# Kernel optimization log

Hardware: AMD Instinct MI355X
Metric: run time of the kernel (lower is better)

The kernel has to match this reference:

```python
import jax, jax.numpy as jnp
import numpy as np

RRELU_SLOPE = (1.0 / 8.0 + 1.0 / 3.0) / 2.0  # F.rrelu deterministic (eval) slope

N_ENTS, H_DIM, R2, T, E = 50000, 200, 500, 4, 400000


def setup_inputs() -> dict:
    key = jax.random.key(0)
    ks = jax.random.split(key, 16)
    s = 0.05
    inp = {
        # learned parameters
        "dynamic_emb": jax.random.normal(ks[0], (N_ENTS, H_DIM), jnp.float32),
        "emb_rel": jax.random.normal(ks[1], (R2, H_DIM), jnp.float32) * s,
        "W_ih": jax.random.normal(ks[2], (3 * H_DIM, 2 * H_DIM), jnp.float32) * s,
        "W_hh": jax.random.normal(ks[3], (3 * H_DIM, H_DIM), jnp.float32) * s,
        "b_ih": jnp.zeros((3 * H_DIM,), jnp.float32),
        "b_hh": jnp.zeros((3 * H_DIM,), jnp.float32),
        "weight_neighbor": jax.random.normal(ks[4], (H_DIM, H_DIM), jnp.float32) * s,
        "time_gate_weight": jax.random.normal(ks[5], (H_DIM, H_DIM), jnp.float32) * s,
        "time_gate_bias": jnp.zeros((H_DIM,), jnp.float32),
        # per-timestep graph structure [T, E]
        "src": jax.random.randint(ks[6], (T, E), 0, N_ENTS, jnp.int32),
        "dst": jax.random.randint(ks[7], (T, E), 0, N_ENTS, jnp.int32),
        "etype": jax.random.randint(ks[8], (T, E), 0, R2, jnp.int32),
        "r_to_e": jax.random.randint(ks[9], (T, E), 0, N_ENTS, jnp.int32),
        "r_seg": jnp.sort(jax.random.randint(ks[10], (T, E), 0, R2, jnp.int32), axis=1),
    }
    return inp


def _l2norm(x):
    # torch F.normalize along dim=1
    return x / jnp.maximum(jnp.linalg.norm(x, axis=1, keepdims=True), 1e-12)


def reference(dynamic_emb, emb_rel, W_ih, W_hh, b_ih, b_hh, weight_neighbor,
              time_gate_weight, time_gate_bias, src, dst, etype, r_to_e, r_seg):
    N, H = dynamic_emb.shape
    R2_ = emb_rel.shape[0]

    def gru(x, hprev):
        gi = x @ W_ih.T + b_ih
        gh = hprev @ W_hh.T + b_hh
        ir, iz, inn = jnp.split(gi, 3, axis=1)
        hr, hz, hn = jnp.split(gh, 3, axis=1)
        r = jax.nn.sigmoid(ir + hr)
        z = jax.nn.sigmoid(iz + hz)
        n = jnp.tanh(inn + r * hn)
        return (1.0 - z) * n + z * hprev

    def rgcn(h, s, d, et):
        # UnionRGCNLayer: msg = (h_src + rel_emb[etype]) @ W_neighbor, sum-agg, 1/deg norm, rrelu
        msg = (h[s] + emb_rel[et]) @ weight_neighbor  # [E, H]
        agg = jax.ops.segment_sum(msg, d, num_segments=N)
        deg = jax.ops.segment_sum(jnp.ones((s.shape[0],), h.dtype), d, num_segments=N)
        norm = jnp.where(deg > 0, 1.0 / jnp.maximum(deg, 1.0), 0.0)
        out = agg * norm[:, None]
        return jnp.where(out >= 0, out, RRELU_SLOPE * out)

    h_init = _l2norm(dynamic_emb)  # layer_norm=True

    def step(carry, g):
        h, h0 = carry
        s, d, et, rte, rseg = g
        # ragged per-relation segment mean of entity embeddings
        temp = h[rte]  # [E, H]
        sums = jax.ops.segment_sum(temp, rseg, num_segments=R2_)
        cnts = jax.ops.segment_sum(jnp.ones((rte.shape[0],), h.dtype), rseg, num_segments=R2_)
        x_input = jnp.where(cnts[:, None] > 0, sums / jnp.maximum(cnts, 1.0)[:, None], 0.0)
        x_cat = jnp.concatenate([emb_rel, x_input], axis=1)  # [R2, 2H]
        h0_new = _l2norm(gru(x_cat, h0))
        cur = _l2norm(rgcn(h, s, d, et))
        tw = jax.nn.sigmoid(h @ time_gate_weight + time_gate_bias)
        h_new = _l2norm(tw * cur + (1.0 - tw) * h)
        return (h_new, h0_new), h_new

    (h_fin, h0_fin), evolve = jax.lax.scan(
        step, (h_init, emb_rel), (src, dst, etype, r_to_e, r_seg))
    return evolve, h0_fin  # evolve: [T, N, H]; h0: [2*num_rels, H]
```

## Files before the change

### kernel.cpp

```cpp
#include <hip/hip_runtime.h>
#include <hip/hip_bf16.h>

using bf16 = __hip_bfloat16;

constexpr int NE  = 50000;
constexpr int H   = 200;
constexpr int R2C = 500;
constexpr int TS  = 4;
constexpr int EC  = 400000;
constexpr float SLOPE = 0.22916666666666666f;
constexpr int NSCAN = (NE + 255) / 256;

constexpr int KP = 224;
constexpr int KS = 7;
constexpr int NT = 13;

constexpr int GNT = 38;
constexpr int GKI = 13;
constexpr int GKH = 7;
constexpr int GR  = 512;
constexpr int GCS = 608;

constexpr int RCH = 64;
constexpr int NRNG = 8;
constexpr int DRNG = NE / NRNG;
constexpr int SCHK = 1024;
constexpr int NCHK = (EC + SCHK - 1) / SCHK;
constexpr int GSCAT1 = NCHK * NRNG;

constexpr int GB_GEMM  = (NE + 63) / 64;
constexpr int GB_RELS  = EC / RCH;
constexpr int GB_AGG   = (NE + 3) / 4;
constexpr int GB_A2B   = (GR * 416 + GR * 224 + 255) / 256;

constexpr int PB_INITH  = (NE + 3) / 4;
constexpr int PB_INITH0 = (R2C * H + 255) / 256;
constexpr int PB_RELW   = R2C;
constexpr int PB_PACKB  = (2 * NT * KS * 64 + 255) / 256;
constexpr int PB_PACKG  = (GNT * (GKI + GKH) * 64 + 255) / 256;
constexpr int PB_SEGB   = TS;
constexpr int PB_ZS     = (TS * R2C * H + 255) / 256;
constexpr int PB_ZI     = (TS * NE + 255) / 256;
constexpr int PO0 = PB_INITH;
constexpr int PO1 = PO0 + PB_INITH0;
constexpr int PO2 = PO1 + PB_RELW;
constexpr int PO3 = PO2 + PB_PACKB;
constexpr int PO4 = PO3 + PB_PACKG;
constexpr int PO5 = PO4 + PB_SEGB;
constexpr int PO6 = PO5 + PB_ZS;
constexpr int PO7 = PO6 + PB_ZI;

#define DEVINL __device__ __forceinline__

typedef __bf16 bf16x8v __attribute__((ext_vector_type(8)));
typedef float  f32x4   __attribute__((ext_vector_type(4)));

DEVINL float b2f(bf16 v) { return __bfloat162float(v); }
DEVINL bf16  f2b(float v) { return __float2bfloat16(v); }
DEVINL unsigned short f2bu(float x) { bf16 b = f2b(x); return *reinterpret_cast<unsigned short*>(&b); }
DEVINL float u2f(unsigned short u) { unsigned int w = (unsigned int)u << 16; float f; __builtin_memcpy(&f, &w, 4); return f; }

DEVINL float wave_sum(float v) {
  #pragma unroll
  for (int o = 32; o > 0; o >>= 1) v += __shfl_xor(v, o, 64);
  return v;
}

DEVINL float sigmoidf(float x) { return 1.0f / (1.0f + expf(-x)); }


DEVINL void inith_body(int b, const float* __restrict__ de, float* __restrict__ h,
                       unsigned short* __restrict__ hb0) {
  int wid = threadIdx.x >> 6, lane = threadIdx.x & 63;
  int row = b * 4 + wid;
  if (row >= NE) return;
  int d0 = lane * 4;
  bool act = d0 < H;
  float4 v = make_float4(0.f, 0.f, 0.f, 0.f);
  if (act) v = *reinterpret_cast<const float4*>(de + (size_t)row * H + d0);
  float ss = v.x * v.x + v.y * v.y + v.z * v.z + v.w * v.w;
  ss = wave_sum(ss);
  float sc = 1.0f / fmaxf(sqrtf(ss), 1e-12f);
  if (act) {
    float4 o = make_float4(v.x * sc, v.y * sc, v.z * sc, v.w * sc);
    *reinterpret_cast<float4*>(h + (size_t)row * H + d0) = o;
    ushort4 ob; ob.x = f2bu(o.x); ob.y = f2bu(o.y); ob.z = f2bu(o.z); ob.w = f2bu(o.w);
    *reinterpret_cast<ushort4*>(hb0 + (size_t)row * KP + d0) = ob;
  } else if (d0 < KP) {
    ushort4 z; z.x = z.y = z.z = z.w = 0;
    *reinterpret_cast<ushort4*>(hb0 + (size_t)row * KP + d0) = z;
  }
}

DEVINL void inith0_body(int b, const float* er, float* h0) {
  int i = b * 256 + threadIdx.x;
  if (i < R2C * H) h0[i] = er[i];
}

DEVINL void relw_body(int b, const float* er, const float* wn, unsigned short* relWb) {
  __shared__ float a[H];
  int r = b;
  for (int d = threadIdx.x; d < H; d += 256) a[d] = er[r * H + d];
  __syncthreads();
  for (int c = threadIdx.x; c < H; c += 256) {
    float s = 0.f;
    for (int k = 0; k < H; k++) s += a[k] * wn[k * H + c];
    relWb[r * H + c] = f2bu(s);
  }
}

DEVINL void packb_body(int b, const float* wn, const float* tg, unsigned short* bpack) {
  int t = b * 256 + threadIdx.x;
  int total = 2 * NT * KS * 64;
  if (t >= total) return;
  int m    = t / (NT * KS * 64);
  int rem  = t % (NT * KS * 64);
  int nt   = rem / (KS * 64);
  int rem2 = rem % (KS * 64);
  int ks   = rem2 / 64, lane = rem2 % 64;
  const float* W = m ? tg : wn;
  int n = nt * 16 + (lane & 15);
  unsigned short out[8];
  #pragma unroll
  for (int j = 0; j < 8; j++) {
    int k = ks * 32 + (lane >> 4) * 8 + j;
    float v = (k < H && n < H) ? W[k * H + n] : 0.f;
    out[j] = f2bu(v);
  }
  unsigned short* dst = bpack + (size_t)t * 8;
  #pragma unroll
  for (int j = 0; j < 8; j++) dst[j] = out[j];
}

DEVINL void packgru_body(int b, const float* __restrict__ wih, const float* __restrict__ whh,
                         unsigned short* __restrict__ bgi, unsigned short* __restrict__ bgh) {
  int t = b * 256 + threadIdx.x;
  const int tot_i = GNT * GKI * 64;
  const int tot_h = GNT * GKH * 64;
  if (t < tot_i) {
    int nt = t / (GKI * 64);
    int rem = t % (GKI * 64);
    int ks = rem / 64, lane = rem % 64;
    int n = nt * 16 + (lane & 15);
    unsigned short o[8];
    #pragma unroll
    for (int j = 0; j < 8; j++) {
      int k = ks * 32 + (lane >> 4) * 8 + j;
      o[j] = (n < 3 * H && k < 2 * H) ? f2bu(wih[n * (2 * H) + k]) : (unsigned short)0;
    }
    unsigned short* dstp = bgi + (size_t)t * 8;
    #pragma unroll
    for (int j = 0; j < 8; j++) dstp[j] = o[j];
  } else if (t < tot_i + tot_h) {
    int t2 = t - tot_i;
    int nt = t2 / (GKH * 64);
    int rem = t2 % (GKH * 64);
    int ks = rem / 64, lane = rem % 64;
    int n = nt * 16 + (lane & 15);
    unsigned short o[8];
    #pragma unroll
    for (int j = 0; j < 8; j++) {
      int k = ks * 32 + (lane >> 4) * 8 + j;
      o[j] = (n < 3 * H && k < H) ? f2bu(whh[n * H + k]) : (unsigned short)0;
    }
    unsigned short* dstp = bgh + (size_t)t2 * 8;
    #pragma unroll
    for (int j = 0; j < 8; j++) dstp[j] = o[j];
  }
}

DEVINL void segb_body(int b, const int* __restrict__ rseg, int* __restrict__ segstart4) {
  const int* rs = rseg + (size_t)b * EC;
  int* out = segstart4 + b * (R2C + 1);
  for (int r = threadIdx.x; r <= R2C; r += 256) {
    int lo = 0, hi = EC;
    while (lo < hi) { int m = (lo + hi) >> 1; if (rs[m] < r) lo = m + 1; else hi = m; }
    out[r] = lo;
  }
}

__global__ __launch_bounds__(256) void k_prologue(const float* __restrict__ de,
                                                  float* __restrict__ h,
                                                  unsigned short* __restrict__ hb0,
                                                  const float* __restrict__ er,
                                                  float* __restrict__ h0,
                                                  const float* __restrict__ wn,
                                                  unsigned short* __restrict__ relWb,
                                                  const float* __restrict__ tg,
                                                  unsigned short* __restrict__ bpack,
                                                  const float* __restrict__ wih,
                                                  const float* __restrict__ whh,
                                                  unsigned short* __restrict__ bgi,
                                                  unsigned short* __restrict__ bgh,
                                                  const int* __restrict__ rseg,
                                                  int* __restrict__ segstart4,
                                                  float* __restrict__ sums4,
                                                  int* __restrict__ deg4) {
  int b = blockIdx.x;
  if (b < PO0)       inith_body(b, de, h, hb0);
  else if (b < PO1)  inith0_body(b - PO0, er, h0);
  else if (b < PO2)  relw_body(b - PO1, er, wn, relWb);
  else if (b < PO3)  packb_body(b - PO2, wn, tg, bpack);
  else if (b < PO4)  packgru_body(b - PO3, wih, whh, bgi, bgh);
  else if (b < PO5)  segb_body(b - PO4, rseg, segstart4);
  else if (b < PO6) { int i = (b - PO5) * 256 + threadIdx.x; if (i < TS * R2C * H) sums4[i] = 0.f; }
  else              { int i = (b - PO6) * 256 + threadIdx.x; if (i < TS * NE) deg4[i] = 0; }
}


__global__ void k_hist4(const int* __restrict__ dst, int* __restrict__ deg4) {
  int base = (blockIdx.x * 256 + threadIdx.x) * 4;
  if (base + 3 < TS * EC) {
    int4 d4 = *reinterpret_cast<const int4*>(dst + base);
    int t = base / EC;
    atomicAdd(&deg4[t * NE + d4.x], 1);
    atomicAdd(&deg4[t * NE + d4.y], 1);
    atomicAdd(&deg4[t * NE + d4.z], 1);
    atomicAdd(&deg4[t * NE + d4.w], 1);
  }
}

__global__ __launch_bounds__(256) void k_scan1(const int* __restrict__ deg4,
                                               int* __restrict__ offs4,
                                               int* __restrict__ bsums4) {
  __shared__ int s[256];
  int t = blockIdx.x / NSCAN, blk = blockIdx.x % NSCAN;
  int i = blk * 256 + threadIdx.x;
  int v = (i < NE) ? deg4[t * NE + i] : 0;
  s[threadIdx.x] = v;
  __syncthreads();
  for (int o = 1; o < 256; o <<= 1) {
    int add = (threadIdx.x >= o) ? s[threadIdx.x - o] : 0;
    __syncthreads();
    s[threadIdx.x] += add;
    __syncthreads();
  }
  if (i < NE) offs4[t * (NE + 1) + i] = s[threadIdx.x] - v;
  if (threadIdx.x == 255) bsums4[t * 256 + blk] = s[255];
}

__global__ __launch_bounds__(256) void k_scan2(int* bsums4) {
  __shared__ int s[256];
  int t = blockIdx.x;
  int v = (threadIdx.x < NSCAN) ? bsums4[t * 256 + threadIdx.x] : 0;
  s[threadIdx.x] = v;
  __syncthreads();
  for (int o = 1; o < 256; o <<= 1) {
    int add = (threadIdx.x >= o) ? s[threadIdx.x - o] : 0;
    __syncthreads();
    s[threadIdx.x] += add;
    __syncthreads();
  }
  if (threadIdx.x < NSCAN) bsums4[t * 256 + threadIdx.x] = s[threadIdx.x] - v;
}

__global__ void k_scan3(int* __restrict__ offs4, const int* __restrict__ bsums4,
                        int* __restrict__ cursor4) {
  int t = blockIdx.x / NSCAN, blk = blockIdx.x % NSCAN;
  int i = blk * 256 + threadIdx.x;
  if (i < NE) {
    int o = offs4[t * (NE + 1) + i] + bsums4[t * 256 + blk];
    offs4[t * (NE + 1) + i] = o;
    cursor4[t * NE + i] = o;
  }
  if (blk == 0 && threadIdx.x == 0) offs4[t * (NE + 1) + NE] = EC;
}


DEVINL void scatter_body(int b, int t, const int* __restrict__ dst, const int* __restrict__ src,
                         const int* __restrict__ et, int* __restrict__ cursor4,
                         unsigned int* __restrict__ se4) {
  int r = b & (NRNG - 1);
  int chunk = b >> 3;
  int li = chunk * SCHK + threadIdx.x * 4;
  if (li >= EC) return;
  int base = t * EC + li;
  int4 d4 = *reinterpret_cast<const int4*>(dst + base);
  int4 s4 = *reinterpret_cast<const int4*>(src + base);
  int4 e4 = *reinterpret_cast<const int4*>(et + base);
  int* cur = cursor4 + t * NE;
  unsigned int* se = se4 + (size_t)t * EC;
  if ((unsigned)d4.x / DRNG == (unsigned)r) {
    int p = atomicAdd(&cur[d4.x], 1);
    se[p] = (unsigned int)s4.x | ((unsigned int)e4.x << 16);
  }
  if ((unsigned)d4.y / DRNG == (unsigned)r) {
    int p = atomicAdd(&cur[d4.y], 1);
    se[p] = (unsigned int)s4.y | ((unsigned int)e4.y << 16);
  }
  if ((unsigned)d4.z / DRNG == (unsigned)r) {
    int p = atomicAdd(&cur[d4.z], 1);
    se[p] = (unsigned int)s4.z | ((unsigned int)e4.z << 16);
  }
  if ((unsigned)d4.w / DRNG == (unsigned)r) {
    int p = atomicAdd(&cur[d4.w], 1);
    se[p] = (unsigned int)s4.w | ((unsigned int)e4.w << 16);
  }
}

DEVINL void relsums_body(int b, const int* __restrict__ rseg, const int* __restrict__ rte,
                         const unsigned short* __restrict__ hb, float* __restrict__ sums) {
  int base = b * RCH;
  int d = threadIdx.x;
  bool act = d < H;
  float a0 = 0.f, a1 = 0.f, a2 = 0.f, a3 = 0.f;
  int prev = rseg[base];
  for (int g = 0; g < RCH; g += 8) {
    int e = base + g;
    int4 sgA = *reinterpret_cast<const int4*>(rseg + e);
    int4 sgB = *reinterpret_cast<const int4*>(rseg + e + 4);
    int4 rrA = *reinterpret_cast<const int4*>(rte + e);
    int4 rrB = *reinterpret_cast<const int4*>(rte + e + 4);
    if (sgB.w == prev) {
      if (act) {
        float v0 = u2f(hb[(size_t)rrA.x * KP + d]);
        float v1 = u2f(hb[(size_t)rrA.y * KP + d]);
        float v2 = u2f(hb[(size_t)rrA.z * KP + d]);
        float v3 = u2f(hb[(size_t)rrA.w * KP + d]);
        float v4 = u2f(hb[(size_t)rrB.x * KP + d]);
        float v5 = u2f(hb[(size_t)rrB.y * KP + d]);
        float v6 = u2f(hb[(size_t)rrB.z * KP + d]);
        float v7 = u2f(hb[(size_t)rrB.w * KP + d]);
        a0 += v0; a1 += v1; a2 += v2; a3 += v3;
        a0 += v4; a1 += v5; a2 += v6; a3 += v7;
      }
    } else {
      int ss[8] = {sgA.x, sgA.y, sgA.z, sgA.w, sgB.x, sgB.y, sgB.z, sgB.w};
      int rr[8] = {rrA.x, rrA.y, rrA.z, rrA.w, rrB.x, rrB.y, rrB.z, rrB.w};
      #pragma unroll
      for (int j = 0; j < 8; j++) {
        if (ss[j] != prev) {
          if (act) atomicAdd(&sums[prev * H + d], a0 + a1 + a2 + a3);
          a0 = a1 = a2 = a3 = 0.f;
          prev = ss[j];
        }
        if (act) a0 += u2f(hb[(size_t)rr[j] * KP + d]);
      }
    }
  }
  if (act) atomicAdd(&sums[prev * H + d], a0 + a1 + a2 + a3);
}

DEVINL void gemm_body(int b, const unsigned short* __restrict__ hb,
                      const unsigned short* __restrict__ bpack,
                      const float* __restrict__ tgb,
                      bf16* __restrict__ hWb, bf16* __restrict__ twb) {
  int wid = threadIdx.x >> 6, lane = threadIdx.x & 63;
  int row0 = b * 64 + wid * 16;
  if (row0 >= NE) return;
  int arow = min(row0 + (lane & 15), NE - 1);
  const unsigned short* ap = hb + (size_t)arow * KP + (lane >> 4) * 8;
  bf16x8v a[KS];
  #pragma unroll
  for (int ks = 0; ks < KS; ks++)
    a[ks] = *reinterpret_cast<const bf16x8v*>(ap + ks * 32);

  const unsigned short* b1p = bpack + (size_t)lane * 8;
  const unsigned short* b2p = b1p + (size_t)NT * KS * 64 * 8;
  int colb = lane & 15;
  int rbase = row0 + (lane >> 4) * 4;

  for (int nt = 0; nt < NT; nt++) {
    bf16x8v b1[KS], b2[KS];
    #pragma unroll
    for (int ks = 0; ks < KS; ks++) {
      size_t boff = (size_t)(nt * KS + ks) * 64 * 8;
      b1[ks] = *reinterpret_cast<const bf16x8v*>(b1p + boff);
      b2[ks] = *reinterpret_cast<const bf16x8v*>(b2p + boff);
    }
    f32x4 acc1 = {}, acc2 = {};
    #pragma unroll
    for (int ks = 0; ks < KS; ks++) {
      acc1 = __builtin_amdgcn_mfma_f32_16x16x32_bf16(a[ks], b1[ks], acc1, 0, 0, 0);
      acc2 = __builtin_amdgcn_mfma_f32_16x16x32_bf16(a[ks], b2[ks], acc2, 0, 0, 0);
    }
    int col = nt * 16 + colb;
    bool cok = (col < H);
    float bias = cok ? tgb[col] : 0.f;
    #pragma unroll
    for (int q = 0; q < 4; q++) {
      int row = rbase + q;
      if (cok && row < NE) {
        hWb[(size_t)row * H + col] = f2b(acc1[q]);
        twb[(size_t)row * H + col] = f2b(sigmoidf(acc2[q] + bias));
      }
    }
  }
}

DEVINL void aggfin_body(int b, const int* __restrict__ offs,
                        const unsigned int* __restrict__ se,
                        const bf16* __restrict__ hWb,
                        const unsigned short* __restrict__ relWb,
                        const bf16* __restrict__ twb,
                        float* __restrict__ h, float* __restrict__ evolve,
                        unsigned short* __restrict__ hbnext) {
  int wid = threadIdx.x >> 6, lane = threadIdx.x & 63;
  int i = b * 4 + wid;
  if (i >= NE) return;
  int s0 = offs[i], s1 = offs[i + 1];
  int d0 = lane * 4;
  bool act = d0 < H;
  const unsigned short* hw = (const unsigned short*)hWb;
  float a0 = 0.f, a1 = 0.f, a2 = 0.f, a3 = 0.f;

  int p = s0;
  for (; p + 4 <= s1; p += 4) {
    unsigned int e0 = se[p], e1 = se[p + 1], e2 = se[p + 2], e3 = se[p + 3];
    if (act) {
      ushort4 m0 = *reinterpret_cast<const ushort4*>(hw + (size_t)(e0 & 0xFFFFu) * H + d0);
      ushort4 m1 = *reinterpret_cast<const ushort4*>(hw + (size_t)(e1 & 0xFFFFu) * H + d0);
      ushort4 m2 = *reinterpret_cast<const ushort4*>(hw + (size_t)(e2 & 0xFFFFu) * H + d0);
      ushort4 m3 = *reinterpret_cast<const ushort4*>(hw + (size_t)(e3 & 0xFFFFu) * H + d0);
      ushort4 r0 = *reinterpret_cast<const ushort4*>(relWb + (size_t)(e0 >> 16) * H + d0);
      ushort4 r1 = *reinterpret_cast<const ushort4*>(relWb + (size_t)(e1 >> 16) * H + d0);
      ushort4 r2 = *reinterpret_cast<const ushort4*>(relWb + (size_t)(e2 >> 16) * H + d0);
      ushort4 r3 = *reinterpret_cast<const ushort4*>(relWb + (size_t)(e3 >> 16) * H + d0);
      a0 += u2f(m0.x) + u2f(r0.x) + u2f(m1.x) + u2f(r1.x)
          + u2f(m2.x) + u2f(r2.x) + u2f(m3.x) + u2f(r3.x);
      a1 += u2f(m0.y) + u2f(r0.y) + u2f(m1.y) + u2f(r1.y)
          + u2f(m2.y) + u2f(r2.y) + u2f(m3.y) + u2f(r3.y);
      a2 += u2f(m0.z) + u2f(r0.z) + u2f(m1.z) + u2f(r1.z)
          + u2f(m2.z) + u2f(r2.z) + u2f(m3.z) + u2f(r3.z);
      a3 += u2f(m0.w) + u2f(r0.w) + u2f(m1.w) + u2f(r1.w)
          + u2f(m2.w) + u2f(r2.w) + u2f(m3.w) + u2f(r3.w);
    }
  }
  for (; p < s1; p++) {
    unsigned int e0 = se[p];
    if (act) {
      ushort4 m0 = *reinterpret_cast<const ushort4*>(hw + (size_t)(e0 & 0xFFFFu) * H + d0);
      ushort4 r0 = *reinterpret_cast<const ushort4*>(relWb + (size_t)(e0 >> 16) * H + d0);
      a0 += u2f(m0.x) + u2f(r0.x);
      a1 += u2f(m0.y) + u2f(r0.y);
      a2 += u2f(m0.z) + u2f(r0.z);
      a3 += u2f(m0.w) + u2f(r0.w);
    }
  }

  int deg = s1 - s0;
  float nrm = deg > 0 ? 1.0f / (float)deg : 0.0f;
  float c0 = a0 * nrm; c0 = c0 >= 0.f ? c0 : SLOPE * c0;
  float c1 = a1 * nrm; c1 = c1 >= 0.f ? c1 : SLOPE * c1;
  float c2 = a2 * nrm; c2 = c2 >= 0.f ? c2 : SLOPE * c2;
  float c3 = a3 * nrm; c3 = c3 >= 0.f ? c3 : SLOPE * c3;
  float ss = act ? (c0 * c0 + c1 * c1 + c2 * c2 + c3 * c3) : 0.f;
  ss = wave_sum(ss);
  float sc = 1.0f / fmaxf(sqrtf(ss), 1e-12f);
  c0 *= sc; c1 *= sc; c2 *= sc; c3 *= sc;

  float v0 = 0.f, v1 = 0.f, v2 = 0.f, v3 = 0.f;
  if (act) {
    ushort4 t4 = *reinterpret_cast<const ushort4*>((const unsigned short*)twb + (size_t)i * H + d0);
    float4 hv = *reinterpret_cast<const float4*>(h + (size_t)i * H + d0);
    float t0 = u2f(t4.x), t1 = u2f(t4.y), t2 = u2f(t4.z), t3 = u2f(t4.w);
    v0 = t0 * c0 + (1.0f - t0) * hv.x;
    v1 = t1 * c1 + (1.0f - t1) * hv.y;
    v2 = t2 * c2 + (1.0f - t2) * hv.z;
    v3 = t3 * c3 + (1.0f - t3) * hv.w;
  }
  float ss2 = v0 * v0 + v1 * v1 + v2 * v2 + v3 * v3;
  ss2 = wave_sum(ss2);
  float sc2 = 1.0f / fmaxf(sqrtf(ss2), 1e-12f);
  if (act) {
    float4 o = make_float4(v0 * sc2, v1 * sc2, v2 * sc2, v3 * sc2);
    *reinterpret_cast<float4*>(h + (size_t)i * H + d0) = o;
    *reinterpret_cast<float4*>(evolve + (size_t)i * H + d0) = o;
    if (hbnext) {
      ushort4 ob; ob.x = f2bu(o.x); ob.y = f2bu(o.y); ob.z = f2bu(o.z); ob.w = f2bu(o.w);
      *reinterpret_cast<ushort4*>(hbnext + (size_t)i * KP + d0) = ob;
    }
  } else if (d0 < KP && hbnext) {
    ushort4 z; z.x = z.y = z.z = z.w = 0;
    *reinterpret_cast<ushort4*>(hbnext + (size_t)i * KP + d0) = z;
  }
}

DEVINL void a2b_body(int b, const float* __restrict__ er, const float* __restrict__ sums,
                     const int* __restrict__ segstart, const float* __restrict__ h0,
                     unsigned short* __restrict__ xcatb, unsigned short* __restrict__ h0b) {
  int i = b * 256 + threadIdx.x;
  const int n1 = GR * 416;
  if (i < n1) {
    int r = i / 416, c = i % 416;
    float v = 0.f;
    if (r < R2C) {
      if (c < H) v = er[r * H + c];
      else if (c < 2 * H) {
        int cnt = segstart[r + 1] - segstart[r];
        float inv = cnt > 0 ? 1.0f / (float)cnt : 0.0f;
        v = sums[r * H + (c - H)] * inv;
      }
    }
    xcatb[i] = f2bu(v);
  } else {
    int i2 = i - n1;
    if (i2 < GR * 224) {
      int r = i2 / 224, c = i2 % 224;
      float v = (r < R2C && c < H) ? h0[r * H + c] : 0.f;
      h0b[i2] = f2bu(v);
    }
  }
}

__global__ __launch_bounds__(256) void k_rsgemm(int t,
                                                const int* __restrict__ rseg,
                                                const int* __restrict__ rte,
                                                const unsigned short* __restrict__ hb,
                                                float* __restrict__ sums,
                                                const unsigned short* __restrict__ bpack,
                                                const float* __restrict__ tgb,
                                                bf16* __restrict__ hWb,
                                                bf16* __restrict__ twb,
                                                const int* __restrict__ dst,
                                                const int* __restrict__ src,
                                                const int* __restrict__ et,
                                                int* __restrict__ cursor4,
                                                unsigned int* __restrict__ se4) {
  int b = blockIdx.x;
  if (b < GB_GEMM)
    gemm_body(b, hb, bpack, tgb, hWb, twb);
  else if (b < GB_GEMM + GB_RELS)
    relsums_body(b - GB_GEMM, rseg, rte, hb, sums);
  else
    scatter_body(b - (GB_GEMM + GB_RELS), t, dst, src, et, cursor4, se4);
}

__global__ __launch_bounds__(256) void k_afa2b(const int* __restrict__ offs,
                                               const unsigned int* __restrict__ se,
                                               const bf16* __restrict__ hWb,
                                               const unsigned short* __restrict__ relWb,
                                               const bf16* __restrict__ twb,
                                               float* __restrict__ h,
                                               float* __restrict__ evolve,
                                               unsigned short* __restrict__ hbnext,
                                               const float* __restrict__ er,
                                               const float* __restrict__ sums,
                                               const int* __restrict__ segstart,
                                               const float* __restrict__ h0,
                                               unsigned short* __restrict__ xcatb,
                                               unsigned short* __restrict__ h0b) {
  if (blockIdx.x < GB_AGG)
    aggfin_body(blockIdx.x, offs, se, hWb, relWb, twb, h, evolve, hbnext);
  else
    a2b_body(blockIdx.x - GB_AGG, er, sums, segstart, h0, xcatb, h0b);
}

__global__ __launch_bounds__(256) void k_grumm(const unsigned short* __restrict__ xcatb,
                                               const unsigned short* __restrict__ h0b,
                                               const unsigned short* __restrict__ bgi,
                                               const unsigned short* __restrict__ bgh,
                                               float* __restrict__ gi_ws,
                                               float* __restrict__ gh_ws) {
  int wid = threadIdx.x >> 6, lane = threadIdx.x & 63;
  int nt   = blockIdx.x % GNT;
  int row0 = (blockIdx.x / GNT) * 64 + wid * 16;
  int arow = row0 + (lane & 15);

  const unsigned short* api = xcatb + (size_t)arow * 416 + (lane >> 4) * 8;
  bf16x8v ai[GKI];
  #pragma unroll
  for (int ks = 0; ks < GKI; ks++)
    ai[ks] = *reinterpret_cast<const bf16x8v*>(api + ks * 32);
  const unsigned short* aph = h0b + (size_t)arow * 224 + (lane >> 4) * 8;
  bf16x8v ah[GKH];
  #pragma unroll
  for (int ks = 0; ks < GKH; ks++)
    ah[ks] = *reinterpret_cast<const bf16x8v*>(aph + ks * 32);

  const unsigned short* bip = bgi + ((size_t)(nt * GKI) * 64 + lane) * 8;
  bf16x8v bi[GKI];
  #pragma unroll
  for (int ks = 0; ks < GKI; ks++)
    bi[ks] = *reinterpret_cast<const bf16x8v*>(bip + (size_t)ks * 64 * 8);
  const unsigned short* bhp = bgh + ((size_t)(nt * GKH) * 64 + lane) * 8;
  bf16x8v bh[GKH];
  #pragma unroll
  for (int ks = 0; ks < GKH; ks++)
    bh[ks] = *reinterpret_cast<const bf16x8v*>(bhp + (size_t)ks * 64 * 8);

  f32x4 a1 = {}, a2 = {};
  #pragma unroll
  for (int ks = 0; ks < GKI; ks++)
    a1 = __builtin_amdgcn_mfma_f32_16x16x32_bf16(ai[ks], bi[ks], a1, 0, 0, 0);
  #pragma unroll
  for (int ks = 0; ks < GKH; ks++)
    a2 = __builtin_amdgcn_mfma_f32_16x16x32_bf16(ah[ks], bh[ks], a2, 0, 0, 0);

  int col = nt * 16 + (lane & 15);
  int rb = row0 + (lane >> 4) * 4;
  #pragma unroll
  for (int q = 0; q < 4; q++) {
    gi_ws[(size_t)(rb + q) * GCS + col] = a1[q];
    gh_ws[(size_t)(rb + q) * GCS + col] = a2[q];
  }
}

__global__ __launch_bounds__(256) void k_grutail(const float* __restrict__ gi_ws,
                                                 const float* __restrict__ gh_ws,
                                                 const float* __restrict__ b_ih,
                                                 const float* __restrict__ b_hh,
                                                 float* __restrict__ h0,
                                                 float* __restrict__ h0_out) {
  __shared__ float xc[H];
  __shared__ float red[4];
  int r = blockIdx.x;
  int tid = threadIdx.x, wid = tid >> 6, lane = tid & 63;
  float ssp = 0.f;
  for (int d = tid; d < H; d += 256) {
    float gir = gi_ws[(size_t)r * GCS + d]         + b_ih[d];
    float ghr = gh_ws[(size_t)r * GCS + d]         + b_hh[d];
    float giz = gi_ws[(size_t)r * GCS + H + d]     + b_ih[H + d];
    float ghz = gh_ws[(size_t)r * GCS + H + d]     + b_hh[H + d];
    float gin = gi_ws[(size_t)r * GCS + 2 * H + d] + b_ih[2 * H + d];
    float ghn = gh_ws[(size_t)r * GCS + 2 * H + d] + b_hh[2 * H + d];
    float rg = sigmoidf(gir + ghr);
    float z  = sigmoidf(giz + ghz);
    float n  = tanhf(gin + rg * ghn);
    float hv = h0[r * H + d];
    float o  = (1.0f - z) * n + z * hv;
    xc[d] = o;
    ssp += o * o;
  }
  ssp = wave_sum(ssp);
  if (lane == 0) red[wid] = ssp;
  __syncthreads();
  float ss = red[0] + red[1] + red[2] + red[3];
  float sc = 1.0f / fmaxf(sqrtf(ss), 1e-12f);
  for (int d = tid; d < H; d += 256) {
    float o = xc[d] * sc;
    h0[r * H + d] = o;
    if (h0_out) h0_out[r * H + d] = o;
  }
}

extern "C" void kernel_launch(void* const* d_in, const int* in_sizes, int n_in,
                              void* d_out, int out_size, void* d_ws, size_t ws_size,
                              hipStream_t stream) {
  const float* de  = (const float*)d_in[0];
  const float* er  = (const float*)d_in[1];
  const float* wih = (const float*)d_in[2];
  const float* whh = (const float*)d_in[3];
  const float* bih = (const float*)d_in[4];
  const float* bhh = (const float*)d_in[5];
  const float* wn  = (const float*)d_in[6];
  const float* tg  = (const float*)d_in[7];
  const float* tgb = (const float*)d_in[8];
  const int* src  = (const int*)d_in[9];
  const int* dst  = (const int*)d_in[10];
  const int* et   = (const int*)d_in[11];
  const int* rte  = (const int*)d_in[12];
  const int* rseg = (const int*)d_in[13];

  char* w = (char*)d_ws;
  auto alloc = [&](size_t bytes) -> char* {
    char* p = w;
    w += (bytes + 255) / 256 * 256;
    return p;
  };
  float* h     = (float*)alloc(sizeof(float) * (size_t)NE * H);
  bf16*  hWb   = (bf16*) alloc(sizeof(bf16)  * (size_t)NE * H);
  bf16*  twb   = (bf16*) alloc(sizeof(bf16)  * (size_t)NE * H);
  unsigned short* relWb = (unsigned short*)alloc(sizeof(unsigned short) * R2C * H);
  float* h0    = (float*)alloc(sizeof(float) * R2C * H);
  float* sums4 = (float*)alloc(sizeof(float) * TS * R2C * H);
  unsigned short* bpack = (unsigned short*)alloc(sizeof(unsigned short) * 2 * NT * KS * 64 * 8);
  unsigned short* bgi   = (unsigned short*)alloc(sizeof(unsigned short) * GNT * GKI * 64 * 8);
  unsigned short* bgh   = (unsigned short*)alloc(sizeof(unsigned short) * GNT * GKH * 64 * 8);
  unsigned short* xcatb = (unsigned short*)alloc(sizeof(unsigned short) * GR * 416);
  unsigned short* h0b   = (unsigned short*)alloc(sizeof(unsigned short) * GR * 224);
  float* gi_ws = (float*)alloc(sizeof(float) * GR * GCS);
  float* gh_ws = (float*)alloc(sizeof(float) * GR * GCS);
  int* segstart4 = (int*)alloc(sizeof(int) * TS * (R2C + 1));
  int* deg4    = (int*) alloc(sizeof(int) * TS * NE);
  int* offs4   = (int*) alloc(sizeof(int) * TS * (NE + 1));
  int* cursor4 = (int*) alloc(sizeof(int) * TS * NE);
  unsigned int* se4 = (unsigned int*)alloc(sizeof(unsigned int) * (size_t)TS * EC);
  int* bsums4  = (int*) alloc(sizeof(int) * TS * 256);
  (void)ws_size; (void)in_sizes; (void)n_in; (void)out_size;

  float* out    = (float*)d_out;
  float* evolve = out;
  float* h0out  = out + (size_t)TS * NE * H;

  const int gGru   = 8 * GNT;
  const int gE4i   = (TS * EC / 4 + 255) / 256;

  k_prologue<<<PO7, 256, 0, stream>>>(de, h, (unsigned short*)evolve, er, h0,
                                      wn, relWb, tg, bpack, wih, whh, bgi, bgh,
                                      rseg, segstart4, sums4, deg4);
  k_hist4<<<gE4i, 256, 0, stream>>>(dst, deg4);
  k_scan1<<<TS * NSCAN, 256, 0, stream>>>(deg4, offs4, bsums4);
  k_scan2<<<TS, 256, 0, stream>>>(bsums4);
  k_scan3<<<TS * NSCAN, 256, 0, stream>>>(offs4, bsums4, cursor4);

  for (int t = 0; t < TS; t++) {
    const int* rseg_t = rseg + (size_t)t * EC;
    const int* rte_t  = rte  + (size_t)t * EC;
    float* sums_t = sums4 + (size_t)t * R2C * H;
    float* evo_t = evolve + (size_t)t * NE * H;
    unsigned short* hb = (unsigned short*)evo_t;
    unsigned short* hbnext = (t < TS - 1) ? (unsigned short*)(evolve + (size_t)(t + 1) * NE * H)
                                          : (unsigned short*)nullptr;

    k_rsgemm<<<GB_GEMM + GB_RELS + GSCAT1, 256, 0, stream>>>(
        t, rseg_t, rte_t, hb, sums_t, bpack, tgb, hWb, twb,
        dst, src, et, cursor4, se4);

    k_afa2b<<<GB_AGG + GB_A2B, 256, 0, stream>>>(offs4 + t * (NE + 1), se4 + (size_t)t * EC,
                                                 hWb, relWb, twb, h, evo_t, hbnext,
                                                 er, sums_t, segstart4 + t * (R2C + 1),
                                                 h0, xcatb, h0b);

    k_grumm<<<gGru, 256, 0, stream>>>(xcatb, h0b, bgi, bgh, gi_ws, gh_ws);
    k_grutail<<<R2C, 256, 0, stream>>>(gi_ws, gh_ws, bih, bhh,
                                       h0, (t == TS - 1) ? h0out : (float*)nullptr);
  }
}
```

Baseline: 674.5 us.

## Replace fp32 state buffer with bf16 ping-pong and defer GRU tail into next step

Removes the fp32 copy of the entity state. The time-gate blend now reads the previous state from padded bf16 ping-pong buffers instead of the fp32 h array, which cuts read and write traffic per step. The GRU tail for each step is folded into the next step's combined rsgemm launch as extra blocks, with one standalone tail launch after the loop, saving kernel launches. In exchange the blend uses bf16-rounded previous state, which slightly reduces accuracy.

```diff
diff --git a/kernel.cpp b/kernel.cpp
--- a/kernel.cpp
+++ b/kernel.cpp
@@ -69,7 +69,7 @@
 DEVINL float sigmoidf(float x) { return 1.0f / (1.0f + expf(-x)); }
 
 
-DEVINL void inith_body(int b, const float* __restrict__ de, float* __restrict__ h,
+DEVINL void inith_body(int b, const float* __restrict__ de,
                        unsigned short* __restrict__ hb0) {
   int wid = threadIdx.x >> 6, lane = threadIdx.x & 63;
   int row = b * 4 + wid;
@@ -81,14 +81,15 @@
   float ss = v.x * v.x + v.y * v.y + v.z * v.z + v.w * v.w;
   ss = wave_sum(ss);
   float sc = 1.0f / fmaxf(sqrtf(ss), 1e-12f);
-  if (act) {
-    float4 o = make_float4(v.x * sc, v.y * sc, v.z * sc, v.w * sc);
-    *reinterpret_cast<float4*>(h + (size_t)row * H + d0) = o;
-    ushort4 ob; ob.x = f2bu(o.x); ob.y = f2bu(o.y); ob.z = f2bu(o.z); ob.w = f2bu(o.w);
+  if (d0 < KP) {
+    ushort4 ob;
+    if (act) {
+      ob.x = f2bu(v.x * sc); ob.y = f2bu(v.y * sc);
+      ob.z = f2bu(v.z * sc); ob.w = f2bu(v.w * sc);
+    } else {
+      ob.x = ob.y = ob.z = ob.w = 0;
+    }
     *reinterpret_cast<ushort4*>(hb0 + (size_t)row * KP + d0) = ob;
-  } else if (d0 < KP) {
-    ushort4 z; z.x = z.y = z.z = z.w = 0;
-    *reinterpret_cast<ushort4*>(hb0 + (size_t)row * KP + d0) = z;
   }
 }
 
@@ -180,7 +181,6 @@
 }
 
 __global__ __launch_bounds__(256) void k_prologue(const float* __restrict__ de,
-                                                  float* __restrict__ h,
                                                   unsigned short* __restrict__ hb0,
                                                   const float* __restrict__ er,
                                                   float* __restrict__ h0,
@@ -197,7 +197,7 @@
                                                   float* __restrict__ sums4,
                                                   int* __restrict__ deg4) {
   int b = blockIdx.x;
-  if (b < PO0)       inith_body(b, de, h, hb0);
+  if (b < PO0)       inith_body(b, de, hb0);
   else if (b < PO1)  inith0_body(b - PO0, er, h0);
   else if (b < PO2)  relw_body(b - PO1, er, wn, relWb);
   else if (b < PO3)  packb_body(b - PO2, wn, tg, bpack);
@@ -388,12 +388,50 @@
   }
 }
 
+DEVINL void grutail_body(int r, const float* __restrict__ gi_ws,
+                         const float* __restrict__ gh_ws,
+                         const float* __restrict__ b_ih,
+                         const float* __restrict__ b_hh,
+                         float* __restrict__ h0,
+                         float* __restrict__ h0_out) {
+  __shared__ float xc[H];
+  __shared__ float red[4];
+  int tid = threadIdx.x, wid = tid >> 6, lane = tid & 63;
+  float ssp = 0.f;
+  for (int d = tid; d < H; d += 256) {
+    float gir = gi_ws[(size_t)r * GCS + d]         + b_ih[d];
+    float ghr = gh_ws[(size_t)r * GCS + d]         + b_hh[d];
+    float giz = gi_ws[(size_t)r * GCS + H + d]     + b_ih[H + d];
+    float ghz = gh_ws[(size_t)r * GCS + H + d]     + b_hh[H + d];
+    float gin = gi_ws[(size_t)r * GCS + 2 * H + d] + b_ih[2 * H + d];
+    float ghn = gh_ws[(size_t)r * GCS + 2 * H + d] + b_hh[2 * H + d];
+    float rg = sigmoidf(gir + ghr);
+    float z  = sigmoidf(giz + ghz);
+    float n  = tanhf(gin + rg * ghn);
+    float hv = h0[r * H + d];
+    float o  = (1.0f - z) * n + z * hv;
+    xc[d] = o;
+    ssp += o * o;
+  }
+  ssp = wave_sum(ssp);
+  if (lane == 0) red[wid] = ssp;
+  __syncthreads();
+  float ss = red[0] + red[1] + red[2] + red[3];
+  float sc = 1.0f / fmaxf(sqrtf(ss), 1e-12f);
+  for (int d = tid; d < H; d += 256) {
+    float o = xc[d] * sc;
+    h0[r * H + d] = o;
+    if (h0_out) h0_out[r * H + d] = o;
+  }
+}
+
 DEVINL void aggfin_body(int b, const int* __restrict__ offs,
                         const unsigned int* __restrict__ se,
                         const bf16* __restrict__ hWb,
                         const unsigned short* __restrict__ relWb,
                         const bf16* __restrict__ twb,
-                        float* __restrict__ h, float* __restrict__ evolve,
+                        const unsigned short* __restrict__ hbcur,
+                        float* __restrict__ evolve,
                         unsigned short* __restrict__ hbnext) {
   int wid = threadIdx.x >> 6, lane = threadIdx.x & 63;
   int i = b * 4 + wid;
@@ -452,19 +490,18 @@
   float v0 = 0.f, v1 = 0.f, v2 = 0.f, v3 = 0.f;
   if (act) {
     ushort4 t4 = *reinterpret_cast<const ushort4*>((const unsigned short*)twb + (size_t)i * H + d0);
-    float4 hv = *reinterpret_cast<const float4*>(h + (size_t)i * H + d0);
+    ushort4 h4 = *reinterpret_cast<const ushort4*>(hbcur + (size_t)i * KP + d0);
     float t0 = u2f(t4.x), t1 = u2f(t4.y), t2 = u2f(t4.z), t3 = u2f(t4.w);
-    v0 = t0 * c0 + (1.0f - t0) * hv.x;
-    v1 = t1 * c1 + (1.0f - t1) * hv.y;
-    v2 = t2 * c2 + (1.0f - t2) * hv.z;
-    v3 = t3 * c3 + (1.0f - t3) * hv.w;
+    v0 = t0 * c0 + (1.0f - t0) * u2f(h4.x);
+    v1 = t1 * c1 + (1.0f - t1) * u2f(h4.y);
+    v2 = t2 * c2 + (1.0f - t2) * u2f(h4.z);
+    v3 = t3 * c3 + (1.0f - t3) * u2f(h4.w);
   }
   float ss2 = v0 * v0 + v1 * v1 + v2 * v2 + v3 * v3;
   ss2 = wave_sum(ss2);
   float sc2 = 1.0f / fmaxf(sqrtf(ss2), 1e-12f);
   if (act) {
     float4 o = make_float4(v0 * sc2, v1 * sc2, v2 * sc2, v3 * sc2);
-    *reinterpret_cast<float4*>(h + (size_t)i * H + d0) = o;
     *reinterpret_cast<float4*>(evolve + (size_t)i * H + d0) = o;
     if (hbnext) {
       ushort4 ob; ob.x = f2bu(o.x); ob.y = f2bu(o.y); ob.z = f2bu(o.z); ob.w = f2bu(o.w);
@@ -516,14 +553,22 @@
                                                 const int* __restrict__ src,
                                                 const int* __restrict__ et,
                                                 int* __restrict__ cursor4,
-                                                unsigned int* __restrict__ se4) {
+                                                unsigned int* __restrict__ se4,
+                                                const float* __restrict__ gi_ws,
+                                                const float* __restrict__ gh_ws,
+                                                const float* __restrict__ b_ih,
+                                                const float* __restrict__ b_hh,
+                                                float* __restrict__ h0) {
   int b = blockIdx.x;
   if (b < GB_GEMM)
     gemm_body(b, hb, bpack, tgb, hWb, twb);
   else if (b < GB_GEMM + GB_RELS)
     relsums_body(b - GB_GEMM, rseg, rte, hb, sums);
+  else if (b < GB_GEMM + GB_RELS + GSCAT1)
+    scatter_body(b - (GB_GEMM + GB_RELS), t, dst, src, et, cursor4, se4);
   else
-    scatter_body(b - (GB_GEMM + GB_RELS), t, dst, src, et, cursor4, se4);
+    grutail_body(b - (GB_GEMM + GB_RELS + GSCAT1), gi_ws, gh_ws, b_ih, b_hh, h0,
+                 (float*)nullptr);
 }
 
 __global__ __launch_bounds__(256) void k_afa2b(const int* __restrict__ offs,
@@ -531,7 +576,7 @@
                                                const bf16* __restrict__ hWb,
                                                const unsigned short* __restrict__ relWb,
                                                const bf16* __restrict__ twb,
-                                               float* __restrict__ h,
+                                               const unsigned short* __restrict__ hbcur,
                                                float* __restrict__ evolve,
                                                unsigned short* __restrict__ hbnext,
                                                const float* __restrict__ er,
@@ -541,7 +586,7 @@
                                                unsigned short* __restrict__ xcatb,
                                                unsigned short* __restrict__ h0b) {
   if (blockIdx.x < GB_AGG)
-    aggfin_body(blockIdx.x, offs, se, hWb, relWb, twb, h, evolve, hbnext);
+    aggfin_body(blockIdx.x, offs, se, hWb, relWb, twb, hbcur, evolve, hbnext);
   else
     a2b_body(blockIdx.x - GB_AGG, er, sums, segstart, h0, xcatb, h0b);
 }
@@ -602,36 +647,7 @@
                                                  const float* __restrict__ b_hh,
                                                  float* __restrict__ h0,
                                                  float* __restrict__ h0_out) {
-  __shared__ float xc[H];
-  __shared__ float red[4];
-  int r = blockIdx.x;
-  int tid = threadIdx.x, wid = tid >> 6, lane = tid & 63;
-  float ssp = 0.f;
-  for (int d = tid; d < H; d += 256) {
-    float gir = gi_ws[(size_t)r * GCS + d]         + b_ih[d];
-    float ghr = gh_ws[(size_t)r * GCS + d]         + b_hh[d];
-    float giz = gi_ws[(size_t)r * GCS + H + d]     + b_ih[H + d];
-    float ghz = gh_ws[(size_t)r * GCS + H + d]     + b_hh[H + d];
-    float gin = gi_ws[(size_t)r * GCS + 2 * H + d] + b_ih[2 * H + d];
-    float ghn = gh_ws[(size_t)r * GCS + 2 * H + d] + b_hh[2 * H + d];
-    float rg = sigmoidf(gir + ghr);
-    float z  = sigmoidf(giz + ghz);
-    float n  = tanhf(gin + rg * ghn);
-    float hv = h0[r * H + d];
-    float o  = (1.0f - z) * n + z * hv;
-    xc[d] = o;
-    ssp += o * o;
-  }
-  ssp = wave_sum(ssp);
-  if (lane == 0) red[wid] = ssp;
-  __syncthreads();
-  float ss = red[0] + red[1] + red[2] + red[3];
-  float sc = 1.0f / fmaxf(sqrtf(ss), 1e-12f);
-  for (int d = tid; d < H; d += 256) {
-    float o = xc[d] * sc;
-    h0[r * H + d] = o;
-    if (h0_out) h0_out[r * H + d] = o;
-  }
+  grutail_body(blockIdx.x, gi_ws, gh_ws, b_ih, b_hh, h0, h0_out);
 }
 
 extern "C" void kernel_launch(void* const* d_in, const int* in_sizes, int n_in,
@@ -658,7 +674,8 @@
     w += (bytes + 255) / 256 * 256;
     return p;
   };
-  float* h     = (float*)alloc(sizeof(float) * (size_t)NE * H);
+  unsigned short* hbA = (unsigned short*)alloc(sizeof(unsigned short) * (size_t)NE * KP);
+  unsigned short* hbB = (unsigned short*)alloc(sizeof(unsigned short) * (size_t)NE * KP);
   bf16*  hWb   = (bf16*) alloc(sizeof(bf16)  * (size_t)NE * H);
   bf16*  twb   = (bf16*) alloc(sizeof(bf16)  * (size_t)NE * H);
   unsigned short* relWb = (unsigned short*)alloc(sizeof(unsigned short) * R2C * H);
@@ -686,7 +703,7 @@
   const int gGru   = 8 * GNT;
   const int gE4i   = (TS * EC / 4 + 255) / 256;
 
-  k_prologue<<<PO7, 256, 0, stream>>>(de, h, (unsigned short*)evolve, er, h0,
+  k_prologue<<<PO7, 256, 0, stream>>>(de, hbA, er, h0,
                                       wn, relWb, tg, bpack, wih, whh, bgi, bgh,
                                       rseg, segstart4, sums4, deg4);
   k_hist4<<<gE4i, 256, 0, stream>>>(dst, deg4);
@@ -699,21 +716,22 @@
     const int* rte_t  = rte  + (size_t)t * EC;
     float* sums_t = sums4 + (size_t)t * R2C * H;
     float* evo_t = evolve + (size_t)t * NE * H;
-    unsigned short* hb = (unsigned short*)evo_t;
-    unsigned short* hbnext = (t < TS - 1) ? (unsigned short*)(evolve + (size_t)(t + 1) * NE * H)
+    unsigned short* hbcur  = (t & 1) ? hbB : hbA;
+    unsigned short* hbnext = (t < TS - 1) ? ((t & 1) ? hbA : hbB)
                                           : (unsigned short*)nullptr;
 
-    k_rsgemm<<<GB_GEMM + GB_RELS + GSCAT1, 256, 0, stream>>>(
-        t, rseg_t, rte_t, hb, sums_t, bpack, tgb, hWb, twb,
-        dst, src, et, cursor4, se4);
+    int nblk = GB_GEMM + GB_RELS + GSCAT1 + (t > 0 ? R2C : 0);
+    k_rsgemm<<<nblk, 256, 0, stream>>>(
+        t, rseg_t, rte_t, hbcur, sums_t, bpack, tgb, hWb, twb,
+        dst, src, et, cursor4, se4, gi_ws, gh_ws, bih, bhh, h0);
 
     k_afa2b<<<GB_AGG + GB_A2B, 256, 0, stream>>>(offs4 + t * (NE + 1), se4 + (size_t)t * EC,
-                                                 hWb, relWb, twb, h, evo_t, hbnext,
+                                                 hWb, relWb, twb, hbcur, evo_t, hbnext,
                                                  er, sums_t, segstart4 + t * (R2C + 1),
                                                  h0, xcatb, h0b);
 
     k_grumm<<<gGru, 256, 0, stream>>>(xcatb, h0b, bgi, bgh, gi_ws, gh_ws);
-    k_grutail<<<R2C, 256, 0, stream>>>(gi_ws, gh_ws, bih, bhh,
-                                       h0, (t == TS - 1) ? h0out : (float*)nullptr);
-  }
-}
+  }
+
+  k_grutail<<<R2C, 256, 0, stream>>>(gi_ws, gh_ws, bih, bhh, h0, h0out);
+}
```

New measurement: 639.8 us (median of 2 runs). 1.05x faster.
